# Kernel tuning notes

Hardware: AMD Instinct MI355X
Metric: run time of the kernel (lower is better)

Reference implementation:

```python
import math
import jax, jax.numpy as jnp
import numpy as np

B, M, N = 32, 64, 5000   # batch, multi_width (POMO rollouts), n_nodes
L, H, D, E = 100, 8, 16, 128  # local_size, head_num, qkv_dim, emb_dim


def setup_inputs() -> dict:
    key = jax.random.key(0)
    ks = jax.random.split(key, 10)
    return {
        "dist": jax.random.uniform(ks[0], (B, M, N), jnp.float32),
        "theta": jax.random.uniform(ks[1], (B, M, N), jnp.float32, minval=-math.pi, maxval=math.pi),
        "ninf_mask": jnp.zeros((B, M, N), jnp.float32),
        "W_init": jax.random.normal(ks[2], (E, 2), jnp.float32) * 0.1,
        "b_init": jax.random.normal(ks[3], (E,), jnp.float32) * 0.1,
        "cur_token": jax.random.uniform(ks[4], (E,), jnp.float32, minval=-1.0, maxval=1.0),
        "Wq": jax.random.normal(ks[5], (H * D, E), jnp.float32) * 0.05,
        "Wk": jax.random.normal(ks[6], (H * D, E), jnp.float32) * 0.05,
        "Wv": jax.random.normal(ks[7], (H * D, E), jnp.float32) * 0.05,
        "Wc": jax.random.normal(ks[8], (E, H * D), jnp.float32) * 0.05,
        "bc": jax.random.normal(ks[9], (E,), jnp.float32) * 0.05,
    }


def _positional_signal():
    # transformer sinusoidal encoding over the L gathered neighbors (E even -> no pad)
    num_ts = E // 2
    log_inc = math.log(10000.0) / max(num_ts - 1, 1)
    inv_ts = jnp.exp(jnp.arange(num_ts, dtype=jnp.float32) * -log_inc)
    pos = jnp.arange(L, dtype=jnp.float32)
    scaled = pos[:, None] * inv_ts[None, :]            # [L, E/2]
    return jnp.concatenate([jnp.sin(scaled), jnp.cos(scaled)], axis=1)  # [L, E]


def reference(dist, theta, ninf_mask, W_init, b_init, cur_token, Wq, Wk, Wv, Wc, bc):
    # mask out infeasible nodes (dist - (-inf) = +inf pushes them out of top-k)
    d = dist - ninf_mask                               # [B, M, N]
    neg_vals, idx = jax.lax.top_k(-d, L)               # smallest-L distances
    sorted_dist = -neg_vals                            # [B, M, L] ascending
    sorted_mask = jnp.take_along_axis(ninf_mask, idx, axis=-1)
    norm = sorted_dist.max(axis=-1, keepdims=True) + 1e-6
    sorted_dist = sorted_dist / norm
    sorted_theta = jnp.take_along_axis(theta, idx, axis=-1)
    sdt = jnp.stack([sorted_dist, sorted_theta], axis=-1)   # [B, M, L, 2]

    init_k = sdt @ W_init.T + b_init + _positional_signal()  # [B, M, L, E]

    # current-token query is a single shared learned vector -> q is [H, D]
    q = (Wq @ cur_token).reshape(H, D)
    kh = (init_k @ Wk.T).reshape(B, M, L, H, D)
    vh = (init_k @ Wv.T).reshape(B, M, L, H, D)

    score = jnp.einsum('hd,bmlhd->bhml', q, kh) / jnp.sqrt(jnp.float32(D))
    score = score + sorted_mask[:, None, :, :]              # rank3 ninf mask
    w = jax.nn.softmax(score, axis=-1)                      # [B, H, M, L]
    att = jnp.einsum('bhml,bmlhd->bmhd', w, vh).reshape(B, M, H * D)
    mh = att @ Wc.T + bc                                    # [B, M, E]

    score2 = jnp.einsum('bme,bmle->bml', mh, init_k) / jnp.sqrt(jnp.float32(E))

    # scatter local scores back into full [B, M, N]
    bi = jnp.arange(B)[:, None, None]
    mi = jnp.arange(M)[None, :, None]
    out = jnp.zeros((B, M, N), jnp.float32).at[bi, mi, idx].set(score2)
    return out
```

## Files before the change

### kernel.cpp

```cpp
#include <hip/hip_runtime.h>
#include <math.h>

#define B_ 32
#define M_ 64
#define N_ 5000
#define L_ 100
#define H_ 8
#define D_ 16
#define E_ 128
#define NI4 1250
#define T0 0.032f
#define CAP 256

#define ST_SD  0
#define ST_TH  128
#define ST_SM  256
#define ST_IX  384
#define ST_S2  512

#define OFF_POSQ  0
#define OFF_C0    800
#define OFF_C1    808
#define OFF_C2    816
#define OFF_PV0   824
#define OFF_PV1   952
#define OFF_PVB   1080
#define OFF_WC0   1208
#define OFF_WC1   1336
#define OFF_WCB   1464
#define OFF_SB    1592
#define OFF_PCB   1596
#define OFF_PV    1696
#define OFF_PCT   14496

__device__ __forceinline__ unsigned int umap(float v) {
  unsigned int b = __float_as_uint(v);
  return (b & 0x80000000u) ? ~b : (b | 0x80000000u);
}
__device__ __forceinline__ float unmap(unsigned int u) {
  unsigned int b = (u & 0x80000000u) ? (u ^ 0x80000000u) : ~u;
  return __uint_as_float(b);
}

__global__ __launch_bounds__(128) void precomp(
    const float* __restrict__ Wq, const float* __restrict__ Wk,
    const float* __restrict__ cur, const float* __restrict__ Wi,
    const float* __restrict__ bi, const float* __restrict__ Wv,
    const float* __restrict__ Wc, const float* __restrict__ bc,
    float* __restrict__ ws)
{
  const int tid = threadIdx.x;
  const int blk = blockIdx.x;
  __shared__ float pr[E_];
  __shared__ float red[8];
  const int lane = tid & 63, wvv = tid >> 6;

  if (blk == 0) {
    float qsv = 0.f;
    for (int e = 0; e < E_; ++e) qsv = fmaf(Wq[tid * E_ + e], cur[e], qsv);
    float wk0=0,wk1=0,wkb=0,pv0=0,pv1=0,pvb=0,wc0=0,wc1=0,wcb=0;
    for (int e = 0; e < E_; ++e) {
      float wi0 = Wi[2*e], wi1 = Wi[2*e+1], bie = bi[e];
      float wk = Wk[tid*E_+e], wvx = Wv[tid*E_+e], wcc = Wc[e*(H_*D_)+tid];
      wk0=fmaf(wk,wi0,wk0);  wk1=fmaf(wk,wi1,wk1);  wkb=fmaf(wk,bie,wkb);
      pv0=fmaf(wvx,wi0,pv0); pv1=fmaf(wvx,wi1,pv1); pvb=fmaf(wvx,bie,pvb);
      wc0=fmaf(wcc,wi0,wc0); wc1=fmaf(wcc,wi1,wc1); wcb=fmaf(wcc,bie,wcb);
    }
    ws[OFF_PV0+tid]=pv0; ws[OFF_PV1+tid]=pv1; ws[OFF_PVB+tid]=pvb;
    ws[OFF_WC0+tid]=wc0; ws[OFF_WC1+tid]=wc1; ws[OFF_WCB+tid]=wcb;
    float c0 = qsv*wk0, c1 = qsv*wk1, c2 = qsv*wkb;
    for (int off = 1; off < 16; off <<= 1) {
      c0 += __shfl_xor(c0, off, 16); c1 += __shfl_xor(c1, off, 16); c2 += __shfl_xor(c2, off, 16);
    }
    if ((tid & 15) == 0) {
      int h = tid >> 4;
      ws[OFF_C0+h] = c0*0.25f; ws[OFF_C1+h] = c1*0.25f; ws[OFF_C2+h] = c2*0.25f;
    }
    float p0 = Wi[2*tid]*bc[tid], p1 = Wi[2*tid+1]*bc[tid], p2 = bi[tid]*bc[tid];
    for (int off = 32; off > 0; off >>= 1) {
      p0 += __shfl_xor(p0, off, 64); p1 += __shfl_xor(p1, off, 64); p2 += __shfl_xor(p2, off, 64);
    }
    if (lane == 0) { red[wvv*3+0]=p0; red[wvv*3+1]=p1; red[wvv*3+2]=p2; }
    __syncthreads();
    if (tid == 0) {
      ws[OFF_SB+0]=red[0]+red[3]; ws[OFF_SB+1]=red[1]+red[4]; ws[OFF_SB+2]=red[2]+red[5];
    }
  } else {
    const int l = blk - 1;
    const float log_inc = 0.14619588050755848f;
    {
      int j = tid & 63;
      float scaled = (float)l * expf(-(float)j * log_inc);
      pr[tid] = (tid < 64) ? sinf(scaled) : cosf(scaled);
    }
    __syncthreads();
    float qsv=0.f, pwk=0.f, accv=0.f, accc=0.f;
    for (int e = 0; e < E_; ++e) qsv = fmaf(Wq[tid*E_+e], cur[e], qsv);
    for (int e = 0; e < E_; ++e) {
      float p = pr[e];
      pwk  = fmaf(Wk[tid*E_+e], p, pwk);
      accv = fmaf(Wv[tid*E_+e], p, accv);
      accc = fmaf(Wc[e*(H_*D_)+tid], p, accc);
    }
    ws[OFF_PV  + l*(H_*D_) + tid] = accv;
    ws[OFF_PCT + tid*L_ + l] = accc;
    float pq = qsv * pwk;
    for (int off = 1; off < 16; off <<= 1) pq += __shfl_xor(pq, off, 16);
    if ((tid & 15) == 0) ws[OFF_POSQ + (tid>>4)*L_ + l] = pq * 0.25f;
    float pb = pr[tid] * bc[tid];
    for (int off = 32; off > 0; off >>= 1) pb += __shfl_xor(pb, off, 64);
    if (lane == 0) red[wvv] = pb;
    __syncthreads();
    if (tid == 0) ws[OFF_PCB + l] = red[0] + red[1];
  }
}

__global__ __launch_bounds__(128, 4) void k1_select(
    const float* __restrict__ dist, const float* __restrict__ theta,
    const float* __restrict__ ninf, float* __restrict__ out)
{
  __shared__ unsigned long long sel[CAP];
  __shared__ unsigned int hist[256];
  __shared__ unsigned int wsum[2];
  __shared__ unsigned int s_cnt, s_chosen, s_cumb2;
  __shared__ float s_nrm;

  const int tid = threadIdx.x;
  const int lane = tid & 63, wv = tid >> 6;
  const size_t base = (size_t)blockIdx.x * N_;
  const float4* d4 = (const float4*)(dist + base);
  const float4* n4 = (const float4*)(ninf + base);

  sel[tid] = ~0ull; sel[tid + 128] = ~0ull;
  if (tid == 0) s_cnt = 0u;
  __syncthreads();

#pragma unroll 2
  for (int t = 0; t < 10; ++t) {
    int i4 = tid + 128 * t;
    if (i4 < NI4) {
      float4 dv = d4[i4], nv = n4[i4];
#pragma unroll
      for (int c = 0; c < 4; ++c) {
        float v = (&dv.x)[c] - (&nv.x)[c];
        if (v < T0) {
          unsigned int p = atomicAdd(&s_cnt, 1u);
          if (p < CAP) sel[p] = ((unsigned long long)umap(v) << 16) | (unsigned)(4 * i4 + c);
        }
      }
    }
  }
  __syncthreads();
  const unsigned int cnt = s_cnt;

  if (cnt < (unsigned)L_ || cnt > (unsigned)CAP) {
    unsigned long long prefix = 0ull;
    unsigned int Krem = L_;
    for (int pass = 0; pass < 6; ++pass) {
      const int shift = 40 - 8 * pass;
      hist[tid] = 0u; hist[tid + 128] = 0u;
      __syncthreads();
      for (int t = 0; t < 10; ++t) {
        int i4 = tid + 128 * t;
        if (i4 < NI4) {
          float4 dv = d4[i4], nv = n4[i4];
#pragma unroll
          for (int c = 0; c < 4; ++c) {
            float v = (&dv.x)[c] - (&nv.x)[c];
            unsigned long long key = ((unsigned long long)umap(v) << 16) | (unsigned)(4 * i4 + c);
            if ((key >> (shift + 8)) == prefix)
              atomicAdd(&hist[(unsigned)(key >> shift) & 0xFFu], 1u);
          }
        }
      }
      __syncthreads();
      unsigned int s0 = hist[2 * tid], s1 = hist[2 * tid + 1];
      unsigned int s = s0 + s1;
      unsigned int v = s;
#pragma unroll
      for (int off = 1; off < 64; off <<= 1) {
        unsigned int x = __shfl_up(v, off, 64);
        if (lane >= off) v += x;
      }
      if (lane == 63) wsum[wv] = v;
      __syncthreads();
      if (wv == 1) v += wsum[0];
      unsigned int cb = v - s;
      if (cb < Krem && v >= Krem) {
        if (cb + s0 >= Krem) { s_chosen = 2u * tid;     s_cumb2 = cb; }
        else                 { s_chosen = 2u * tid + 1; s_cumb2 = cb + s0; }
      }
      __syncthreads();
      prefix = (prefix << 8) | s_chosen;
      Krem -= s_cumb2;
      __syncthreads();
    }
    const unsigned long long kpiv = prefix;
    sel[tid] = ~0ull; sel[tid + 128] = ~0ull;
    if (tid == 0) s_cnt = 0u;
    __syncthreads();
    for (int t = 0; t < 10; ++t) {
      int i4 = tid + 128 * t;
      if (i4 < NI4) {
        float4 dv = d4[i4], nv = n4[i4];
#pragma unroll
        for (int c = 0; c < 4; ++c) {
          float v = (&dv.x)[c] - (&nv.x)[c];
          unsigned long long key = ((unsigned long long)umap(v) << 16) | (unsigned)(4 * i4 + c);
          if (key <= kpiv) {
            unsigned int p = atomicAdd(&s_cnt, 1u);
            if (p < CAP) sel[p] = key;
          }
        }
      }
    }
    __syncthreads();
  }

  {
    unsigned long long ka = sel[tid], kb = sel[tid + 128];
    const bool va = (ka != ~0ull), vb = (kb != ~0ull);
    unsigned int ixa = (unsigned int)(ka & 0xFFFFull);
    unsigned int ixb = (unsigned int)(kb & 0xFFFFull);
    float tha = 0.f, nma = 0.f, thb = 0.f, nmb = 0.f;
    if (va) { tha = theta[base + ixa]; nma = ninf[base + ixa]; }
    if (vb) { thb = theta[base + ixb]; nmb = ninf[base + ixb]; }
    int ra = 0, rb = 0;
#pragma unroll 8
    for (int j = 0; j < CAP; ++j) {
      unsigned long long kj = sel[j];
      ra += (kj < ka) ? 1 : 0;
      rb += (kj < kb) ? 1 : 0;
    }
    float sda = unmap((unsigned int)(ka >> 16));
    float sdb = unmap((unsigned int)(kb >> 16));
    if (va && ra == 99) s_nrm = sda;
    if (vb && rb == 99) s_nrm = sdb;
    __syncthreads();
    const float invn = 1.0f / (s_nrm + 1e-6f);
    if (va && ra < L_) {
      out[base + ST_SD + ra] = sda * invn;
      out[base + ST_TH + ra] = tha;
      out[base + ST_SM + ra] = nma;
      out[base + ST_IX + ra] = __uint_as_float(ixa);
    }
    if (vb && rb < L_) {
      out[base + ST_SD + rb] = sdb * invn;
      out[base + ST_TH + rb] = thb;
      out[base + ST_SM + rb] = nmb;
      out[base + ST_IX + rb] = __uint_as_float(ixb);
    }
  }
}

__global__ __launch_bounds__(128, 4) void k2_math(
    const float* __restrict__ ws, float* __restrict__ out)
{
  __shared__ float sdv[128], stv[128], smv[128];
  __shared__ float att[H_ * D_];

  const int tid = threadIdx.x;
  const size_t base = (size_t)blockIdx.x * N_;

  if (tid < L_) {
    sdv[tid] = out[base + ST_SD + tid];
    stv[tid] = out[base + ST_TH + tid];
    smv[tid] = out[base + ST_SM + tid];
  }
  __syncthreads();

  {
    const int hh = tid >> 4, jj = tid & 15;
    float w7[7];
    float a0, a1;
    const float c0 = ws[OFF_C0 + hh], c1 = ws[OFF_C1 + hh], c2 = ws[OFF_C2 + hh];
    float mx = -INFINITY;
#pragma unroll
    for (int k = 0; k < 7; ++k) {
      int l = jj + 16 * k;
      float scv = -INFINITY;
      if (l < L_)
        scv = fmaf(sdv[l], c0, fmaf(stv[l], c1, c2 + ws[OFF_POSQ + hh * L_ + l] + smv[l]));
      w7[k] = scv;
      mx = fmaxf(mx, scv);
    }
#pragma unroll
    for (int off = 1; off <= 8; off <<= 1) mx = fmaxf(mx, __shfl_xor(mx, off, 64));
    float sum = 0.f;
#pragma unroll
    for (int k = 0; k < 7; ++k) { float e = expf(w7[k] - mx); w7[k] = e; sum += e; }
#pragma unroll
    for (int off = 1; off <= 8; off <<= 1) sum += __shfl_xor(sum, off, 64);
    const float inv = 1.0f / sum;
    a0 = 0.f; a1 = 0.f;
#pragma unroll
    for (int k = 0; k < 7; ++k) {
      int l = jj + 16 * k; int lc = (l < L_) ? l : 0;
      float wgt = w7[k] * inv; w7[k] = wgt;
      a0 = fmaf(wgt, sdv[lc], a0);
      a1 = fmaf(wgt, stv[lc], a1);
    }
#pragma unroll
    for (int off = 1; off <= 8; off <<= 1) { a0 += __shfl_xor(a0, off, 64); a1 += __shfl_xor(a1, off, 64); }
    {
      float part[16];
#pragma unroll
      for (int t = 0; t < 16; ++t) part[t] = 0.f;
#pragma unroll
      for (int k = 0; k < 7; ++k) {
        int l = jj + 16 * k;
        if (l < L_) {
          const float* pv = ws + OFF_PV + l * (H_ * D_) + hh * 16;
          float wgt = w7[k];
#pragma unroll
          for (int t = 0; t < 16; ++t) part[t] = fmaf(wgt, pv[t], part[t]);
        }
      }
#pragma unroll
      for (int off = 1; off <= 8; off <<= 1) {
#pragma unroll
        for (int t = 0; t < 16; ++t) part[t] += __shfl_xor(part[t], off, 64);
      }
#pragma unroll
      for (int t = 0; t < 16; ++t) {
        int hd = hh * 16 + t;
        att[hd] = fmaf(a0, ws[OFF_PV0 + hd], fmaf(a1, ws[OFF_PV1 + hd], ws[OFF_PVB + hd])) + part[t];
      }
    }
  }
  __syncthreads();

  float m0, m1, mb;
  {
    const int lane = tid & 63;
    float x0 = att[lane], x1 = att[lane + 64];
    m0 = fmaf(x0, ws[OFF_WC0 + lane], x1 * ws[OFF_WC0 + lane + 64]);
    m1 = fmaf(x0, ws[OFF_WC1 + lane], x1 * ws[OFF_WC1 + lane + 64]);
    mb = fmaf(x0, ws[OFF_WCB + lane], x1 * ws[OFF_WCB + lane + 64]);
#pragma unroll
    for (int off = 1; off < 64; off <<= 1) {
      m0 += __shfl_xor(m0, off, 64);
      m1 += __shfl_xor(m1, off, 64);
      mb += __shfl_xor(mb, off, 64);
    }
    m0 += ws[OFF_SB + 0]; m1 += ws[OFF_SB + 1]; mb += ws[OFF_SB + 2];
  }

  if (tid < L_) {
    float acc = ws[OFF_PCB + tid];
#pragma unroll 16
    for (int hd = 0; hd < H_ * D_; ++hd) acc = fmaf(att[hd], ws[OFF_PCT + hd * L_ + tid], acc);
    const float SC = 0.08838834764831845f;
    out[base + ST_S2 + tid] = (fmaf(sdv[tid], m0, fmaf(stv[tid], m1, mb)) + acc) * SC;
  }
}

__global__ __launch_bounds__(256, 4) void k3_write(float* __restrict__ out)
{
  __shared__ unsigned int bitmap[160];
  __shared__ unsigned int hidx[256];
  __shared__ float hval[256];

  const int tid = threadIdx.x;
  const size_t base = (size_t)blockIdx.x * N_;

  unsigned int myidx = 0u; float myval = 0.f;
  if (tid < L_) {
    myidx = __float_as_uint(out[base + ST_IX + tid]);
    myval = out[base + ST_S2 + tid];
  }
  hidx[tid] = 0xFFFFFFFFu;
  if (tid < 160) bitmap[tid] = 0u;
  __syncthreads();
  if (tid < L_) {
    unsigned int p = myidx & 255u;
    while (atomicCAS(&hidx[p], 0xFFFFFFFFu, myidx) != 0xFFFFFFFFu) p = (p + 1) & 255u;
    hval[p] = myval;
    atomicOr(&bitmap[myidx >> 5], 1u << (myidx & 31));
  }
  __syncthreads();

  float4* o4 = (float4*)(out + base);
#pragma unroll
  for (int t = 0; t < 5; ++t) {
    int i4 = tid + 256 * t;
    if (i4 < NI4) {
      unsigned int wbits = (bitmap[i4 >> 3] >> ((i4 & 7) * 4)) & 0xFu;
      float4 o = make_float4(0.f, 0.f, 0.f, 0.f);
      if (wbits) {
#pragma unroll
        for (int c = 0; c < 4; ++c) {
          if ((wbits >> c) & 1u) {
            unsigned int idx = (unsigned int)(4 * i4 + c);
            unsigned int p = idx & 255u;
            while (hidx[p] != idx) p = (p + 1) & 255u;
            (&o.x)[c] = hval[p];
          }
        }
      }
      o4[i4] = o;
    }
  }
}

extern "C" void kernel_launch(void* const* d_in, const int* in_sizes, int n_in,
                              void* d_out, int out_size, void* d_ws, size_t ws_size,
                              hipStream_t stream) {
  const float* dist = (const float*)d_in[0];
  const float* theta = (const float*)d_in[1];
  const float* ninf = (const float*)d_in[2];
  const float* Wi   = (const float*)d_in[3];
  const float* bi   = (const float*)d_in[4];
  const float* cur  = (const float*)d_in[5];
  const float* Wq   = (const float*)d_in[6];
  const float* Wk   = (const float*)d_in[7];
  const float* Wv   = (const float*)d_in[8];
  const float* Wc   = (const float*)d_in[9];
  const float* bcv  = (const float*)d_in[10];
  float* out = (float*)d_out;
  float* ws  = (float*)d_ws;

  precomp<<<dim3(L_ + 1), dim3(128), 0, stream>>>(Wq, Wk, cur, Wi, bi, Wv, Wc, bcv, ws);
  k1_select<<<dim3(B_ * M_), dim3(128), 0, stream>>>(dist, theta, ninf, out);
  k2_math<<<dim3(B_ * M_), dim3(128), 0, stream>>>(ws, out);
  k3_write<<<dim3(B_ * M_), dim3(256), 0, stream>>>(out);
}
```

Baseline: 73.49 us.

## Split threshold filter into grid-wide kernel and fuse select, math, scatter per row

Candidate filtering moves into a separate grid-strided kernel. It loads many float4s per thread up front and appends candidates to per-row scratch regions in the output through global atomics. The per-row selection, attention math and scatter-write kernels are merged into one kernel, so intermediates stay in shared memory instead of round-tripping through global memory, and one launch is removed. The trade-offs are contended global atomics in the filter and a larger shared-memory footprint in the fused row kernel. The index packing also shrinks from 16 to 13 bits.

```diff
diff --git a/kernel.cpp b/kernel.cpp
--- a/kernel.cpp
+++ b/kernel.cpp
@@ -9,14 +9,13 @@
 #define D_ 16
 #define E_ 128
 #define NI4 1250
-#define T0 0.032f
+#define NROW (B_ * M_)
+#define NI4T (NROW * NI4)
+#define T0 0.033f
 #define CAP 256
 
-#define ST_SD  0
-#define ST_TH  128
-#define ST_SM  256
-#define ST_IX  384
-#define ST_S2  512
+#define RC_CAND 1024
+#define RC_CNT  4992
 
 #define OFF_POSQ  0
 #define OFF_C0    800
@@ -47,13 +46,19 @@
     const float* __restrict__ cur, const float* __restrict__ Wi,
     const float* __restrict__ bi, const float* __restrict__ Wv,
     const float* __restrict__ Wc, const float* __restrict__ bc,
-    float* __restrict__ ws)
+    float* __restrict__ ws, float* __restrict__ out)
 {
   const int tid = threadIdx.x;
   const int blk = blockIdx.x;
   __shared__ float pr[E_];
   __shared__ float red[8];
   const int lane = tid & 63, wvv = tid >> 6;
+
+  if (blk >= 101) {
+    int r = (blk - 101) * 128 + tid;
+    if (r < NROW) *(unsigned int*)(out + (size_t)r * N_ + RC_CNT) = 0u;
+    return;
+  }
 
   if (blk == 0) {
     float qsv = 0.f;
@@ -115,45 +120,84 @@
   }
 }
 
-__global__ __launch_bounds__(128, 4) void k1_select(
+__global__ __launch_bounds__(256, 4) void k1a_filter(
+    const float* __restrict__ dist, const float* __restrict__ ninf,
+    float* __restrict__ out)
+{
+  const int tg = blockIdx.x * 256 + threadIdx.x;
+  const int STR = NROW * 256;
+  const float4* d4 = (const float4*)dist;
+  const float4* n4 = (const float4*)ninf;
+
+  float4 dr[5], nr[5];
+#pragma unroll
+  for (int k = 0; k < 5; ++k) {
+    int i4 = tg + k * STR;
+    if (i4 < NI4T) { dr[k] = d4[i4]; nr[k] = n4[i4]; }
+  }
+#pragma unroll
+  for (int k = 0; k < 5; ++k) {
+    int i4 = tg + k * STR;
+    if (i4 < NI4T) {
+#pragma unroll
+      for (int c = 0; c < 4; ++c) {
+        float v = (&dr[k].x)[c] - (&nr[k].x)[c];
+        if (v < T0) {
+          int i = 4 * i4 + c;
+          int row = i / N_;
+          int idx = i - row * N_;
+          unsigned int pos = atomicAdd((unsigned int*)(out + (size_t)row * N_ + RC_CNT), 1u);
+          if (pos < CAP) {
+            unsigned int* slot = (unsigned int*)(out + (size_t)row * N_ + RC_CAND + 2 * pos);
+            slot[0] = umap(v);
+            slot[1] = (unsigned int)idx;
+          }
+        }
+      }
+    }
+  }
+}
+
+__global__ __launch_bounds__(128, 4) void k1b_row(
     const float* __restrict__ dist, const float* __restrict__ theta,
-    const float* __restrict__ ninf, float* __restrict__ out)
+    const float* __restrict__ ninf, const float* __restrict__ ws,
+    float* __restrict__ out)
 {
   __shared__ unsigned long long sel[CAP];
   __shared__ unsigned int hist[256];
+  __shared__ float sdv[128], stv[128], smv[128];
+  __shared__ unsigned int idxs[128];
+  __shared__ float att[H_ * D_];
+  __shared__ unsigned int bitmap[160];
+  __shared__ unsigned int hidx[256];
+  __shared__ float hval[256];
   __shared__ unsigned int wsum[2];
-  __shared__ unsigned int s_cnt, s_chosen, s_cumb2;
+  __shared__ unsigned int s_chosen, s_cumb2, s_cnt;
   __shared__ float s_nrm;
 
   const int tid = threadIdx.x;
   const int lane = tid & 63, wv = tid >> 6;
   const size_t base = (size_t)blockIdx.x * N_;
-  const float4* d4 = (const float4*)(dist + base);
-  const float4* n4 = (const float4*)(ninf + base);
-
-  sel[tid] = ~0ull; sel[tid + 128] = ~0ull;
-  if (tid == 0) s_cnt = 0u;
-  __syncthreads();
-
-#pragma unroll 2
-  for (int t = 0; t < 10; ++t) {
-    int i4 = tid + 128 * t;
-    if (i4 < NI4) {
-      float4 dv = d4[i4], nv = n4[i4];
-#pragma unroll
-      for (int c = 0; c < 4; ++c) {
-        float v = (&dv.x)[c] - (&nv.x)[c];
-        if (v < T0) {
-          unsigned int p = atomicAdd(&s_cnt, 1u);
-          if (p < CAP) sel[p] = ((unsigned long long)umap(v) << 16) | (unsigned)(4 * i4 + c);
-        }
-      }
-    }
-  }
-  __syncthreads();
-  const unsigned int cnt = s_cnt;
-
-  if (cnt < (unsigned)L_ || cnt > (unsigned)CAP) {
+
+  const unsigned int cnt = *(const unsigned int*)(out + base + RC_CNT);
+
+  hidx[tid] = 0xFFFFFFFFu; hidx[tid + 128] = 0xFFFFFFFFu;
+  for (int j = tid; j < 160; j += 128) bitmap[j] = 0u;
+
+  if (cnt >= (unsigned)L_ && cnt <= (unsigned)CAP) {
+    const unsigned int* cw = (const unsigned int*)(out + base + RC_CAND);
+    for (int j = tid; j < CAP; j += 128) {
+      unsigned long long k = ~0ull;
+      if (j < (int)cnt) {
+        unsigned int w0 = cw[2 * j], w1 = cw[2 * j + 1];
+        k = ((unsigned long long)w0 << 13) | w1;
+      }
+      sel[j] = k;
+    }
+    __syncthreads();
+  } else {
+    const float4* d4 = (const float4*)(dist + base);
+    const float4* n4 = (const float4*)(ninf + base);
     unsigned long long prefix = 0ull;
     unsigned int Krem = L_;
     for (int pass = 0; pass < 6; ++pass) {
@@ -167,7 +211,7 @@
 #pragma unroll
           for (int c = 0; c < 4; ++c) {
             float v = (&dv.x)[c] - (&nv.x)[c];
-            unsigned long long key = ((unsigned long long)umap(v) << 16) | (unsigned)(4 * i4 + c);
+            unsigned long long key = ((unsigned long long)umap(v) << 13) | (unsigned)(4 * i4 + c);
             if ((key >> (shift + 8)) == prefix)
               atomicAdd(&hist[(unsigned)(key >> shift) & 0xFFu], 1u);
           }
@@ -206,7 +250,7 @@
 #pragma unroll
         for (int c = 0; c < 4; ++c) {
           float v = (&dv.x)[c] - (&nv.x)[c];
-          unsigned long long key = ((unsigned long long)umap(v) << 16) | (unsigned)(4 * i4 + c);
+          unsigned long long key = ((unsigned long long)umap(v) << 13) | (unsigned)(4 * i4 + c);
           if (key <= kpiv) {
             unsigned int p = atomicAdd(&s_cnt, 1u);
             if (p < CAP) sel[p] = key;
@@ -220,8 +264,8 @@
   {
     unsigned long long ka = sel[tid], kb = sel[tid + 128];
     const bool va = (ka != ~0ull), vb = (kb != ~0ull);
-    unsigned int ixa = (unsigned int)(ka & 0xFFFFull);
-    unsigned int ixb = (unsigned int)(kb & 0xFFFFull);
+    unsigned int ixa = (unsigned int)(ka & 0x1FFFull);
+    unsigned int ixb = (unsigned int)(kb & 0x1FFFull);
     float tha = 0.f, nma = 0.f, thb = 0.f, nmb = 0.f;
     if (va) { tha = theta[base + ixa]; nma = ninf[base + ixa]; }
     if (vb) { thb = theta[base + ixb]; nmb = ninf[base + ixb]; }
@@ -232,40 +276,14 @@
       ra += (kj < ka) ? 1 : 0;
       rb += (kj < kb) ? 1 : 0;
     }
-    float sda = unmap((unsigned int)(ka >> 16));
-    float sdb = unmap((unsigned int)(kb >> 16));
-    if (va && ra == 99) s_nrm = sda;
-    if (vb && rb == 99) s_nrm = sdb;
+    float sda = unmap((unsigned int)(ka >> 13));
+    float sdb = unmap((unsigned int)(kb >> 13));
+    if (va && ra == L_ - 1) s_nrm = sda;
+    if (vb && rb == L_ - 1) s_nrm = sdb;
     __syncthreads();
     const float invn = 1.0f / (s_nrm + 1e-6f);
-    if (va && ra < L_) {
-      out[base + ST_SD + ra] = sda * invn;
-      out[base + ST_TH + ra] = tha;
-      out[base + ST_SM + ra] = nma;
-      out[base + ST_IX + ra] = __uint_as_float(ixa);
-    }
-    if (vb && rb < L_) {
-      out[base + ST_SD + rb] = sdb * invn;
-      out[base + ST_TH + rb] = thb;
-      out[base + ST_SM + rb] = nmb;
-      out[base + ST_IX + rb] = __uint_as_float(ixb);
-    }
-  }
-}
-
-__global__ __launch_bounds__(128, 4) void k2_math(
-    const float* __restrict__ ws, float* __restrict__ out)
-{
-  __shared__ float sdv[128], stv[128], smv[128];
-  __shared__ float att[H_ * D_];
-
-  const int tid = threadIdx.x;
-  const size_t base = (size_t)blockIdx.x * N_;
-
-  if (tid < L_) {
-    sdv[tid] = out[base + ST_SD + tid];
-    stv[tid] = out[base + ST_TH + tid];
-    smv[tid] = out[base + ST_SM + tid];
+    if (va && ra < L_) { sdv[ra] = sda * invn; stv[ra] = tha; smv[ra] = nma; idxs[ra] = ixa; }
+    if (vb && rb < L_) { sdv[rb] = sdb * invn; stv[rb] = thb; smv[rb] = nmb; idxs[rb] = ixb; }
   }
   __syncthreads();
 
@@ -332,7 +350,6 @@
 
   float m0, m1, mb;
   {
-    const int lane = tid & 63;
     float x0 = att[lane], x1 = att[lane + 64];
     m0 = fmaf(x0, ws[OFF_WC0 + lane], x1 * ws[OFF_WC0 + lane + 64]);
     m1 = fmaf(x0, ws[OFF_WC1 + lane], x1 * ws[OFF_WC1 + lane + 64]);
@@ -351,39 +368,22 @@
 #pragma unroll 16
     for (int hd = 0; hd < H_ * D_; ++hd) acc = fmaf(att[hd], ws[OFF_PCT + hd * L_ + tid], acc);
     const float SC = 0.08838834764831845f;
-    out[base + ST_S2 + tid] = (fmaf(sdv[tid], m0, fmaf(stv[tid], m1, mb)) + acc) * SC;
-  }
-}
-
-__global__ __launch_bounds__(256, 4) void k3_write(float* __restrict__ out)
-{
-  __shared__ unsigned int bitmap[160];
-  __shared__ unsigned int hidx[256];
-  __shared__ float hval[256];
-
-  const int tid = threadIdx.x;
-  const size_t base = (size_t)blockIdx.x * N_;
-
-  unsigned int myidx = 0u; float myval = 0.f;
-  if (tid < L_) {
-    myidx = __float_as_uint(out[base + ST_IX + tid]);
-    myval = out[base + ST_S2 + tid];
-  }
-  hidx[tid] = 0xFFFFFFFFu;
-  if (tid < 160) bitmap[tid] = 0u;
+    float s2v = (fmaf(sdv[tid], m0, fmaf(stv[tid], m1, mb)) + acc) * SC;
+    unsigned int idx = idxs[tid] & 0x1FFFu;
+    unsigned int p = idx & 255u;
+    for (int probe = 0; probe < 256; ++probe) {
+      if (atomicCAS(&hidx[p], 0xFFFFFFFFu, idx) == 0xFFFFFFFFu) break;
+      p = (p + 1) & 255u;
+    }
+    hval[p] = s2v;
+    if (idx < (unsigned)N_) atomicOr(&bitmap[idx >> 5], 1u << (idx & 31));
+  }
   __syncthreads();
-  if (tid < L_) {
-    unsigned int p = myidx & 255u;
-    while (atomicCAS(&hidx[p], 0xFFFFFFFFu, myidx) != 0xFFFFFFFFu) p = (p + 1) & 255u;
-    hval[p] = myval;
-    atomicOr(&bitmap[myidx >> 5], 1u << (myidx & 31));
-  }
-  __syncthreads();
 
   float4* o4 = (float4*)(out + base);
 #pragma unroll
-  for (int t = 0; t < 5; ++t) {
-    int i4 = tid + 256 * t;
+  for (int t = 0; t < 10; ++t) {
+    int i4 = tid + 128 * t;
     if (i4 < NI4) {
       unsigned int wbits = (bitmap[i4 >> 3] >> ((i4 & 7) * 4)) & 0xFu;
       float4 o = make_float4(0.f, 0.f, 0.f, 0.f);
@@ -393,8 +393,14 @@
           if ((wbits >> c) & 1u) {
             unsigned int idx = (unsigned int)(4 * i4 + c);
             unsigned int p = idx & 255u;
-            while (hidx[p] != idx) p = (p + 1) & 255u;
-            (&o.x)[c] = hval[p];
+            float val = 0.f;
+            for (int probe = 0; probe < 256; ++probe) {
+              unsigned int h = hidx[p];
+              if (h == idx) { val = hval[p]; break; }
+              if (h == 0xFFFFFFFFu) break;
+              p = (p + 1) & 255u;
+            }
+            (&o.x)[c] = val;
           }
         }
       }
@@ -420,8 +426,7 @@
   float* out = (float*)d_out;
   float* ws  = (float*)d_ws;
 
-  precomp<<<dim3(L_ + 1), dim3(128), 0, stream>>>(Wq, Wk, cur, Wi, bi, Wv, Wc, bcv, ws);
-  k1_select<<<dim3(B_ * M_), dim3(128), 0, stream>>>(dist, theta, ninf, out);
-  k2_math<<<dim3(B_ * M_), dim3(128), 0, stream>>>(ws, out);
-  k3_write<<<dim3(B_ * M_), dim3(256), 0, stream>>>(out);
-}
+  precomp<<<dim3(117), dim3(128), 0, stream>>>(Wq, Wk, cur, Wi, bi, Wv, Wc, bcv, ws, out);
+  k1a_filter<<<dim3(NROW), dim3(256), 0, stream>>>(dist, ninf, out);
+  k1b_row<<<dim3(NROW), dim3(128), 0, stream>>>(dist, theta, ninf, ws, out);
+}
```

Result: slower. 100.1 us (+36.1%).
